# Performance work log

Measured on AMD Instinct MI355X. Metric: run time of the kernel, lower is better.

## Reference

```python
import jax, jax.numpy as jnp
import numpy as np

B, T, H, D = 2, 2048, 8, 128
HID = H * D          # 1024
K_CONV = 4
EPS = 1e-5


def causal_dwconv(x, w, b):
    # x: [B,T,C], w: [C,K], b: [C]
    # torch Conv1d(groups=C, padding=K-1) followed by [..., :T] == left-padded causal depthwise conv
    K = w.shape[1]
    Tx = x.shape[1]
    xp = jnp.pad(x, ((0, 0), (K - 1, 0), (0, 0)))
    acc = jnp.zeros_like(x)
    for j in range(K):  # tiny fixed loop over kernel taps
        acc = acc + xp[:, j:j + Tx, :] * w[:, j]
    return acc + b


def setup_inputs() -> dict:
    key = jax.random.key(0)
    ks = jax.random.split(key, 16)
    s = 0.02
    inp = {
        'x':   jax.random.normal(ks[0], (B, T, HID), jnp.float32),
        'Wq':  s * jax.random.normal(ks[1], (HID, H * D), jnp.float32),
        'Wk':  s * jax.random.normal(ks[2], (HID, H * D), jnp.float32),
        'Wv':  s * jax.random.normal(ks[3], (HID, H * D), jnp.float32),
        'Wa':  s * jax.random.normal(ks[4], (HID, H * D), jnp.float32),
        'ba':  jnp.zeros((H * D,), jnp.float32),
        'Wb':  s * jax.random.normal(ks[5], (HID, H), jnp.float32),
        'bb':  jnp.zeros((H,), jnp.float32),
        'Wg':  s * jax.random.normal(ks[6], (HID, H * D), jnp.float32),
        'Wo':  s * jax.random.normal(ks[7], (H * D, HID), jnp.float32),
        'cqw': s * jax.random.normal(ks[8], (H * D, K_CONV), jnp.float32),
        'cqb': jnp.zeros((H * D,), jnp.float32),
        'ckw': s * jax.random.normal(ks[9], (H * D, K_CONV), jnp.float32),
        'ckb': jnp.zeros((H * D,), jnp.float32),
        'cvw': s * jax.random.normal(ks[10], (H * D, K_CONV), jnp.float32),
        'cvb': jnp.zeros((H * D,), jnp.float32),
        'ln_g': jnp.ones((D,), jnp.float32),
        'ln_b': jnp.zeros((D,), jnp.float32),
    }
    return inp


def reference(x, Wq, Wk, Wv, Wa, ba, Wb, bb, Wg, Wo,
              cqw, cqb, ckw, ckb, cvw, cvb, ln_g, ln_b):
    Bx, Tx, _ = x.shape
    q = x @ Wq
    k = x @ Wk
    v = x @ Wv
    q = jax.nn.silu(causal_dwconv(q, cqw, cqb))
    k = jax.nn.silu(causal_dwconv(k, ckw, ckb))
    v = jax.nn.silu(causal_dwconv(v, cvw, cvb))
    q = q.reshape(Bx, Tx, H, D)
    k = k.reshape(Bx, Tx, H, D) * (D ** -0.5)   # k scaled by head_dim_qk**-0.5
    v = v.reshape(Bx, Tx, H, D)
    a = jax.nn.sigmoid(x @ Wa + ba).reshape(Bx, Tx, H, D)
    beta = jax.nn.sigmoid(x @ Wb + bb)           # [B,T,H]

    # delta-rule recurrent scan; state S: [B,H,Dv,Dk]
    def step(S, inp):
        q_t, k_t, v_t, a_t, b_t = inp            # [B,H,D] / beta [B,H]
        delta = jnp.einsum('bhvk,bhk->bhv', S, k_t)
        err = delta - v_t
        S = a_t[..., None] * S - (b_t[..., None] * err)[..., None] * k_t[:, :, None, :]
        o_t = jnp.einsum('bhvk,bhk->bhv', S, q_t)
        return S, o_t

    tfirst = lambda z: jnp.moveaxis(z, 1, 0)     # [B,T,...] -> [T,B,...]
    S0 = jnp.zeros((Bx, H, D, D), x.dtype)
    _, o = jax.lax.scan(step, S0, (tfirst(q), tfirst(k), tfirst(v), tfirst(a), tfirst(beta)))
    o = jnp.moveaxis(o, 0, 1)                    # [B,T,H,D]

    # LayerNorm over head_dim_v
    mu = o.mean(-1, keepdims=True)
    var = ((o - mu) ** 2).mean(-1, keepdims=True)
    o = (o - mu) * jax.lax.rsqrt(var + EPS) * ln_g + ln_b

    g = jax.nn.sigmoid(x @ Wg).reshape(Bx, Tx, H, D)
    o = (o * g).reshape(Bx, Tx, H * D)
    return o @ Wo
```

## Files before the change

### kernel.cpp

```cpp
#include <hip/hip_runtime.h>
#include <hip/hip_bf16.h>
#include <cstdint>
#include <cstddef>

#define BATCH 2
#define TLEN  2048
#define NHEAD 8
#define HD    128
#define HIDN  1024
#define MTOT  4096
#define MAT_ELEMS 1048576
#define XELEMS 4194304
#define SCAN_C 32
#define NCH    64
#define SSC  1024.0f
#define ISSC 0.0009765625f

typedef _Float16 f16;
typedef _Float16 f16x2 __attribute__((ext_vector_type(2)));
typedef _Float16 f16x8 __attribute__((ext_vector_type(8)));
typedef float    f32x4 __attribute__((ext_vector_type(4)));

__device__ __forceinline__ float sigmoidf_(float v) { return 1.0f / (1.0f + __expf(-v)); }

__device__ __forceinline__ float fdot2_(f16x2 a, f16x2 b, float c)
{
#if __has_builtin(__builtin_amdgcn_fdot2)
    return __builtin_amdgcn_fdot2(a, b, c, false);
#else
    return fmaf((float)a.x, (float)b.x, fmaf((float)a.y, (float)b.y, c));
#endif
}

__device__ __forceinline__ void gload_lds16(const f16* g, f16* l)
{
    __builtin_amdgcn_global_load_lds(
        (const __attribute__((address_space(1))) uint32_t*)(g),
        (__attribute__((address_space(3))) uint32_t*)(l), 16, 0, 0);
}

__global__ __launch_bounds__(256) void convert_x_kernel(const float* __restrict__ x,
                                                        f16* __restrict__ x16)
{
    int i = (blockIdx.x * 256 + threadIdx.x) * 4;
    float4 v = *(const float4*)(x + i);
    union { f16 h[4]; uint2 u; } pk;
    pk.h[0] = (f16)v.x; pk.h[1] = (f16)v.y; pk.h[2] = (f16)v.z; pk.h[3] = (f16)v.w;
    *(uint2*)(x16 + i) = pk.u;
}

__global__ __launch_bounds__(256) void transpose_convert_kernel(
    const float* __restrict__ Wq, const float* __restrict__ Wk, const float* __restrict__ Wv,
    const float* __restrict__ Wa, const float* __restrict__ Wg, const float* __restrict__ Wo,
    f16* __restrict__ WT)
{
    __shared__ float tile[32][33];
    int mat = blockIdx.z;
    const float* W = (mat == 0) ? Wq : (mat == 1) ? Wk : (mat == 2) ? Wv
                   : (mat == 3) ? Wa : (mat == 4) ? Wg : Wo;
    int k0 = blockIdx.y * 32, n0 = blockIdx.x * 32;
    int tr = threadIdx.x >> 3;
    int tc = (threadIdx.x & 7) * 4;
    float4 vin = *(const float4*)(W + (size_t)(k0 + tr) * HIDN + n0 + tc);
    tile[tr][tc + 0] = vin.x; tile[tr][tc + 1] = vin.y;
    tile[tr][tc + 2] = vin.z; tile[tr][tc + 3] = vin.w;
    __syncthreads();
    f16* dst = WT + (size_t)(mat * HIDN + n0 + tr) * HIDN + k0 + tc;
    union { f16 h[4]; uint2 u; } pk;
    pk.h[0] = (f16)tile[tc + 0][tr]; pk.h[1] = (f16)tile[tc + 1][tr];
    pk.h[2] = (f16)tile[tc + 2][tr]; pk.h[3] = (f16)tile[tc + 3][tr];
    *(uint2*)dst = pk.u;
}

template <int MODE>
__global__ __launch_bounds__(256) void gemm_f16(
    const f16* __restrict__ A, const f16* __restrict__ BT,
    float* __restrict__ out_f32,
    f16* __restrict__ qkv_hat, float* __restrict__ a_buf, f16* __restrict__ g16,
    const float* __restrict__ ba)
{
    __shared__ __align__(16) f16 As[128][32];
    __shared__ __align__(16) f16 Bs[128][32];
    int m0 = blockIdx.y * 128;
    int n0 = blockIdx.x * 128;
    int tid = threadIdx.x;
    int w = tid >> 6, lane = tid & 63;
    int L16 = lane & 15, quad = lane >> 4;
    int wm = (w >> 1) * 64, wn = (w & 1) * 64;

    f32x4 acc[4][4];
#pragma unroll
    for (int i = 0; i < 4; ++i)
#pragma unroll
        for (int j = 0; j < 4; ++j) acc[i][j] = (f32x4){0.f, 0.f, 0.f, 0.f};

    int ldr = tid >> 2;
    int ldc = (tid & 3) * 8;
    f16* asb0 = &As[0][0]  + w * 512;
    f16* asb1 = &As[64][0] + w * 512;
    f16* bsb0 = &Bs[0][0]  + w * 512;
    f16* bsb1 = &Bs[64][0] + w * 512;

    for (int k0 = 0; k0 < 1024; k0 += 32) {
        __syncthreads();
        gload_lds16(A  + (size_t)(m0 + ldr) * HIDN + k0 + ldc,      asb0);
        gload_lds16(A  + (size_t)(m0 + ldr + 64) * HIDN + k0 + ldc, asb1);
        gload_lds16(BT + (size_t)(n0 + ldr) * HIDN + k0 + ldc,      bsb0);
        gload_lds16(BT + (size_t)(n0 + ldr + 64) * HIDN + k0 + ldc, bsb1);
        __syncthreads();
        f16x8 af[4], bf[4];
#pragma unroll
        for (int i = 0; i < 4; ++i) {
            af[i] = *(const f16x8*)(&As[wm + i * 16 + L16][quad * 8]);
            bf[i] = *(const f16x8*)(&Bs[wn + i * 16 + L16][quad * 8]);
        }
#pragma unroll
        for (int i = 0; i < 4; ++i)
#pragma unroll
            for (int j = 0; j < 4; ++j)
                acc[i][j] = __builtin_amdgcn_mfma_f32_16x16x32_f16(af[i], bf[j], acc[i][j], 0, 0, 0);
    }

#pragma unroll
    for (int i = 0; i < 4; ++i) {
#pragma unroll
        for (int j = 0; j < 4; ++j) {
            f32x4 c = acc[i][j];
            int mbase = m0 + wm + i * 16 + quad * 4;
            int n = n0 + wn + j * 16 + L16;
            if (MODE == 1) {
#pragma unroll
                for (int r = 0; r < 4; ++r)
                    out_f32[(size_t)(mbase + r) * HIDN + n] = c[r];
            } else {
                int mat = n >> 10;
                int nn = n & 1023;
                if (mat < 3) {
#pragma unroll
                    for (int r = 0; r < 4; ++r)
                        qkv_hat[(size_t)mat * XELEMS + (size_t)(mbase + r) * HIDN + nn] = (f16)c[r];
                } else if (mat == 3) {
                    float bav = ba[nn];
#pragma unroll
                    for (int r = 0; r < 4; ++r)
                        a_buf[(size_t)(mbase + r) * HIDN + nn] = sigmoidf_(c[r] + bav);
                } else {
#pragma unroll
                    for (int r = 0; r < 4; ++r)
                        g16[(size_t)(mbase + r) * HIDN + nn] = (f16)sigmoidf_(c[r]);
                }
            }
        }
    }
}

__global__ __launch_bounds__(256) void beta_kernel(const float* __restrict__ x,
                                                   const float* __restrict__ Wb,
                                                   const float* __restrict__ bb,
                                                   float* __restrict__ beta_buf)
{
    int row = blockIdx.x;
    int h = threadIdx.x >> 5, lane = threadIdx.x & 31;
    const float* xr = x + (size_t)row * HIDN;
    float part = 0.f;
    for (int i = lane; i < HIDN; i += 32)
        part += xr[i] * Wb[i * NHEAD + h];
#pragma unroll
    for (int m = 1; m <= 16; m <<= 1) part += __shfl_xor(part, m);
    if (lane == 0)
        beta_buf[(size_t)row * NHEAD + h] = sigmoidf_(part + bb[h]);
}

__global__ __launch_bounds__(256) void conv_silu_kernel(
    const f16* __restrict__ qkv_hat,
    const float* __restrict__ cqw, const float* __restrict__ cqb,
    const float* __restrict__ ckw, const float* __restrict__ ckb,
    const float* __restrict__ cvw, const float* __restrict__ cvb,
    f16* __restrict__ qkv16)
{
    int z = blockIdx.y;
    int row = blockIdx.x;
    int tloc = row & (TLEN - 1);
    int c4 = threadIdx.x * 4;
    const f16* src = qkv_hat + (size_t)z * XELEMS;
    const float* w  = (z == 0) ? cqw : (z == 1) ? ckw : cvw;
    const float* bi = (z == 0) ? cqb : (z == 1) ? ckb : cvb;

    float xv[4][4];
#pragma unroll
    for (int j = 0; j < 4; ++j) {
        int tt = tloc - 3 + j;
        if (tt >= 0) {
            const f16* p = src + (size_t)(row - 3 + j) * HIDN + c4;
            xv[j][0] = (float)p[0]; xv[j][1] = (float)p[1];
            xv[j][2] = (float)p[2]; xv[j][3] = (float)p[3];
        } else {
            xv[j][0] = xv[j][1] = xv[j][2] = xv[j][3] = 0.f;
        }
    }
    float scale = (z == 1) ? 0.08838834764831845f : 1.0f;
    union { f16 h[4]; uint2 u; } pk;
#pragma unroll
    for (int cc = 0; cc < 4; ++cc) {
        float4 wc = *(const float4*)(w + (size_t)(c4 + cc) * 4);
        float acc = bi[c4 + cc] + wc.x * xv[0][cc] + wc.y * xv[1][cc]
                                 + wc.z * xv[2][cc] + wc.w * xv[3][cc];
        pk.h[cc] = (f16)(acc * sigmoidf_(acc) * scale);
    }
    *(uint2*)(qkv16 + (size_t)z * XELEMS + (size_t)row * HIDN + c4) = pk.u;
}

__global__ __launch_bounds__(64) void gram_kernel(
    const f16* __restrict__ q16, const f16* __restrict__ k16,
    f16* __restrict__ G_g, f16* __restrict__ KQ_g,
    f16* __restrict__ Gx_g, f16* __restrict__ Qx_g, f16* __restrict__ KT_g)
{
    int ch = blockIdx.x;
    int bh = blockIdx.y;
    int b = bh >> 3, h = bh & 7;
    int lane = threadIdx.x;
    int L16 = lane & 15, quad = lane >> 4;
    size_t rowbase = (size_t)(b * TLEN) * HIDN + h * HD;
    int t0 = ch * SCAN_C;
    bool hasNext = (ch + 1 < NCH);

    union ZU { uint4 u; f16x8 v; };
    ZU zz; zz.u = (uint4){0, 0, 0, 0};

    f16x8 kc[2][4], qc[2][4], kn[2][4], qn[2][4];
#pragma unroll
    for (int nt = 0; nt < 2; ++nt)
#pragma unroll
        for (int kk = 0; kk < 4; ++kk) {
            size_t g = rowbase + (size_t)(t0 + nt * 16 + L16) * HIDN + kk * 32 + quad * 8;
            kc[nt][kk] = *(const f16x8*)(k16 + g);
            qc[nt][kk] = *(const f16x8*)(q16 + g);
            if (hasNext) {
                kn[nt][kk] = *(const f16x8*)(k16 + g + (size_t)SCAN_C * HIDN);
                qn[nt][kk] = *(const f16x8*)(q16 + g + (size_t)SCAN_C * HIDN);
            } else {
                kn[nt][kk] = zz.v; qn[nt][kk] = zz.v;
            }
        }

    f32x4 aG[2][2], aKQ[2][2], aGx[2][2], aQx[2][2];
#pragma unroll
    for (int i = 0; i < 2; ++i)
#pragma unroll
        for (int j = 0; j < 2; ++j) {
            aG[i][j] = (f32x4){0, 0, 0, 0}; aKQ[i][j] = (f32x4){0, 0, 0, 0};
            aGx[i][j] = (f32x4){0, 0, 0, 0}; aQx[i][j] = (f32x4){0, 0, 0, 0};
        }
#pragma unroll
    for (int kk = 0; kk < 4; ++kk)
#pragma unroll
        for (int mt = 0; mt < 2; ++mt)
#pragma unroll
            for (int nt = 0; nt < 2; ++nt) {
                aG[mt][nt]  = __builtin_amdgcn_mfma_f32_16x16x32_f16(kc[mt][kk], kc[nt][kk], aG[mt][nt], 0, 0, 0);
                aKQ[mt][nt] = __builtin_amdgcn_mfma_f32_16x16x32_f16(kc[mt][kk], qc[nt][kk], aKQ[mt][nt], 0, 0, 0);
                aGx[mt][nt] = __builtin_amdgcn_mfma_f32_16x16x32_f16(kc[mt][kk], kn[nt][kk], aGx[mt][nt], 0, 0, 0);
                aQx[mt][nt] = __builtin_amdgcn_mfma_f32_16x16x32_f16(kc[mt][kk], qn[nt][kk], aQx[mt][nt], 0, 0, 0);
            }

    size_t gb = ((size_t)bh * NCH + ch) * 1024;
#pragma unroll
    for (int nt = 0; nt < 2; ++nt) {
        int t = nt * 16 + L16;
#pragma unroll
        for (int mt = 0; mt < 2; ++mt) {
            union { f16 e[4]; uint2 u2; } pg, pq, px, py;
#pragma unroll
            for (int r = 0; r < 4; ++r) {
                pg.e[r] = (f16)aG[mt][nt][r];
                pq.e[r] = (f16)aKQ[mt][nt][r];
                px.e[r] = (f16)aGx[mt][nt][r];
                py.e[r] = (f16)aQx[mt][nt][r];
            }
            *(uint2*)(G_g  + gb + t * 32 + mt * 16 + quad * 4) = pg.u2;
            *(uint2*)(KQ_g + gb + t * 32 + mt * 16 + quad * 4) = pq.u2;
            *(uint2*)(Gx_g + gb + t * 32 + mt * 16 + quad * 4) = px.u2;
            *(uint2*)(Qx_g + gb + t * 32 + mt * 16 + quad * 4) = py.u2;
        }
    }
    size_t kb = ((size_t)bh * NCH + ch) * 4096;
#pragma unroll
    for (int nt = 0; nt < 2; ++nt) {
        int t = nt * 16 + L16;
#pragma unroll
        for (int kk = 0; kk < 4; ++kk)
#pragma unroll
            for (int j = 0; j < 8; ++j) {
                int k = kk * 32 + quad * 8 + j;
                KT_g[kb + (size_t)k * 32 + t] = kc[nt][kk][j];
            }
    }
}

__global__ __launch_bounds__(128, 1) void scan2_kernel(
    const f16* __restrict__ q16, const f16* __restrict__ k16, const f16* __restrict__ v16,
    const float* __restrict__ a_buf, const float* __restrict__ beta_buf,
    const f16* __restrict__ G_g, const f16* __restrict__ KQ_g,
    const f16* __restrict__ Gx_g, const f16* __restrict__ Qx_g, const f16* __restrict__ KT_g,
    float* __restrict__ o_buf)
{
    __shared__ __align__(16) float Sp[16 * 132];
    __shared__ __align__(16) f16   Sp16[16 * 136];
    __shared__ __align__(16) f16   KT_lds2[2][4096];
    __shared__ __align__(16) f16   G_lds[2][1024];
    __shared__ __align__(16) f16   Q_lds[2][1024];
    __shared__ __align__(16) f16   Gx_lds[2][1024];
    __shared__ __align__(16) f16   Qx_lds[2][1024];
    __shared__ __align__(16) float skv[2][16 * 34];
    __shared__ __align__(16) float sqv[2][16 * 34];
    __shared__ __align__(16) float avb[2][16 * 68];
    __shared__ __align__(16) float Bts[2][32];
    __shared__ __align__(16) f16   c16s[2][16 * 40];
    __shared__ __align__(16) float PCs[2][16];
    __shared__ __align__(16) float o_lds[2][16][34];

    const int tid = threadIdx.x;
    const int wid = tid >> 6;
    const int lane = tid & 63;
    const int L16 = lane & 15, quad = lane >> 4;
    const int vl = lane >> 2, li = lane & 3;
    const int t_av = lane >> 1, halfsel = lane & 1;

    const int bh = blockIdx.x;
    const int b = bh >> 3, h = bh & 7;
    const int v0 = blockIdx.y * 16;
    const size_t rowbase = (size_t)(b * TLEN) * HIDN + h * HD;
    const size_t gmatbase = (size_t)bh * NCH;

    {
        for (int i = tid; i < 16 * 132; i += 128) Sp[i] = 0.f;
        uint32_t* z;
        z = (uint32_t*)Sp16;    for (int i = tid; i < 16 * 136 / 2; i += 128) z[i] = 0u;
        z = (uint32_t*)KT_lds2; for (int i = tid; i < 2 * 4096 / 2; i += 128) z[i] = 0u;
        z = (uint32_t*)G_lds;   for (int i = tid; i < 1024;          i += 128) z[i] = 0u;
        z = (uint32_t*)Q_lds;   for (int i = tid; i < 1024;          i += 128) z[i] = 0u;
        z = (uint32_t*)Gx_lds;  for (int i = tid; i < 1024;          i += 128) z[i] = 0u;
        z = (uint32_t*)Qx_lds;  for (int i = tid; i < 1024;          i += 128) z[i] = 0u;
        z = (uint32_t*)skv;     for (int i = tid; i < 2 * 16 * 34;   i += 128) z[i] = 0u;
        z = (uint32_t*)sqv;     for (int i = tid; i < 2 * 16 * 34;   i += 128) z[i] = 0u;
        z = (uint32_t*)avb;     for (int i = tid; i < 2 * 16 * 68;   i += 128) z[i] = 0u;
        z = (uint32_t*)Bts;     for (int i = tid; i < 2 * 32;        i += 128) z[i] = 0u;
        z = (uint32_t*)c16s;    for (int i = tid; i < 2 * 16 * 40 / 2; i += 128) z[i] = 0u;
        z = (uint32_t*)PCs;     for (int i = tid; i < 2 * 16;        i += 128) z[i] = 0u;
    }
    __syncthreads();

    if (wid == 1) {
        f16x8 kfA[2][4], qfA[2][4], kfB[2][4], qfB[2][4];

        {
            size_t gb0 = gmatbase * 1024;
            *(uint4*)(&G_lds[0][lane * 16])     = *(const uint4*)(G_g  + gb0 + lane * 16);
            *(uint4*)(&G_lds[0][lane * 16 + 8]) = *(const uint4*)(G_g  + gb0 + lane * 16 + 8);
            *(uint4*)(&Q_lds[0][lane * 16])     = *(const uint4*)(KQ_g + gb0 + lane * 16);
            *(uint4*)(&Q_lds[0][lane * 16 + 8]) = *(const uint4*)(KQ_g + gb0 + lane * 16 + 8);
            size_t ga = rowbase + (size_t)t_av * HIDN + v0 + halfsel * 8;
            float4 ar0 = *(const float4*)(a_buf + ga);
            float4 ar1 = *(const float4*)(a_buf + ga + 4);
            uint4  vr  = *(const uint4*)(v16 + ga);
            float betr = beta_buf[((size_t)(b * TLEN) + t_av) * NHEAD + h];
            const f16* vh = (const f16*)&vr;
            const float* aa0 = (const float*)&ar0;
            const float* aa1 = (const float*)&ar1;
#pragma unroll
            for (int e = 0; e < 4; ++e) {
                float2 wv; wv.x = aa0[e]; wv.y = betr * (float)vh[e];
                *(float2*)(&avb[0][(halfsel * 8 + e) * 68 + 2 * t_av]) = wv;
                float2 wu; wu.x = aa1[e]; wu.y = betr * (float)vh[4 + e];
                *(float2*)(&avb[0][(halfsel * 8 + 4 + e) * 68 + 2 * t_av]) = wu;
            }
            if (halfsel == 0) Bts[0][t_av] = betr;
        }
        __syncthreads();

#define DO_UPDATE_MM(KF, QF)                                                        \
        if (ch >= 1 && ch <= NCH - 2) {                                             \
            f16x8 ca = *(const f16x8*)(&c16s[np][L16 * 40 + quad * 8]);             \
            float pc = PCs[np][L16];                                                \
            _Pragma("unroll")                                                       \
            for (int kt = 0; kt < 8; ++kt) {                                        \
                f16x8 bu = *(const f16x8*)(&KT_lds2[p][(kt * 16 + L16) * 32 + quad * 8]); \
                f32x4 d = __builtin_amdgcn_mfma_f32_16x16x32_f16(bu, ca, (f32x4){0, 0, 0, 0}, 0, 0, 0); \
                int idx = L16 * 132 + kt * 16 + quad * 4;                           \
                float4 s = *(const float4*)(&Sp[idx]);                              \
                s.x = fmaf(pc, s.x, d[0]);                                          \
                s.y = fmaf(pc, s.y, d[1]);                                          \
                s.z = fmaf(pc, s.z, d[2]);                                          \
                s.w = fmaf(pc, s.w, d[3]);                                          \
                *(float4*)(&Sp[idx]) = s;                                           \
                union { f16 e[4]; uint2 u2; } ph;                                   \
                ph.e[0] = (f16)s.x; ph.e[1] = (f16)s.y;                             \
                ph.e[2] = (f16)s.z; ph.e[3] = (f16)s.w;                             \
                *(uint2*)(&Sp16[L16 * 136 + kt * 16 + quad * 4]) = ph.u2;           \
            }                                                                       \
            f32x4 accK[2], accQ[2];                                                 \
            accK[0] = (f32x4){0, 0, 0, 0}; accK[1] = (f32x4){0, 0, 0, 0};           \
            accQ[0] = (f32x4){0, 0, 0, 0}; accQ[1] = (f32x4){0, 0, 0, 0};           \
            _Pragma("unroll")                                                       \
            for (int kk = 0; kk < 4; ++kk) {                                        \
                f16x8 sf = *(const f16x8*)(&Sp16[L16 * 136 + kk * 32 + quad * 8]);  \
                _Pragma("unroll")                                                   \
                for (int nt = 0; nt < 2; ++nt) {                                    \
                    accK[nt] = __builtin_amdgcn_mfma_f32_16x16x32_f16(sf, KF[nt][kk], accK[nt], 0, 0, 0); \
                    accQ[nt] = __builtin_amdgcn_mfma_f32_16x16x32_f16(sf, QF[nt][kk], accQ[nt], 0, 0, 0); \
                }                                                                   \
            }                                                                       \
            _Pragma("unroll")                                                       \
            for (int nt = 0; nt < 2; ++nt) {                                        \
                int t = nt * 16 + L16;                                              \
                _Pragma("unroll")                                                   \
                for (int r = 0; r < 4; ++r) {                                       \
                    skv[np][(quad * 4 + r) * 34 + t] = accK[nt][r];                 \
                    sqv[np][(quad * 4 + r) * 34 + t] = accQ[nt][r];                 \
                }                                                                   \
            }                                                                       \
        }

#define DO_PREFETCH(KF, QF)                                                         \
        if (ch <= NCH - 3) {                                                        \
            int tp = (ch + 2) * SCAN_C;                                             \
            _Pragma("unroll")                                                       \
            for (int nt = 0; nt < 2; ++nt)                                          \
                _Pragma("unroll")                                                   \
                for (int kk = 0; kk < 4; ++kk) {                                    \
                    size_t g = rowbase + (size_t)(tp + nt * 16 + L16) * HIDN + kk * 32 + quad * 8; \
                    KF[nt][kk] = *(const f16x8*)(k16 + g);                          \
                    QF[nt][kk] = *(const f16x8*)(q16 + g);                          \
                }                                                                   \
        }

        for (int ch = 0; ch < NCH; ++ch) {
            const int p = ch & 1;
            const int np = p ^ 1;
            const bool haveNext = (ch + 1 < NCH);

            float4 ar0, ar1; uint4 vr; float betr = 0.f;
            if (haveNext) {
                size_t gbn = (gmatbase + ch + 1) * 1024;
                size_t gbc = (gmatbase + ch) * 1024;
                const f16* gG = G_g  + gbn + lane * 8;
                const f16* gQ = KQ_g + gbn + lane * 8;
                const f16* gX = Gx_g + gbc + lane * 8;
                const f16* gY = Qx_g + gbc + lane * 8;
                gload_lds16(gG,       &G_lds[np][0]);
                gload_lds16(gG + 512, &G_lds[np][512]);
                gload_lds16(gQ,       &Q_lds[np][0]);
                gload_lds16(gQ + 512, &Q_lds[np][512]);
                gload_lds16(gX,       &Gx_lds[np][0]);
                gload_lds16(gX + 512, &Gx_lds[np][512]);
                gload_lds16(gY,       &Qx_lds[np][0]);
                gload_lds16(gY + 512, &Qx_lds[np][512]);
                const f16* gK = KT_g + (gmatbase + ch) * 4096 + lane * 8;
#pragma unroll
                for (int i = 0; i < 8; ++i)
                    gload_lds16(gK + i * 512, &KT_lds2[np][i * 512]);
                int tn = (ch + 1) * SCAN_C;
                size_t ga = rowbase + (size_t)(tn + t_av) * HIDN + v0 + halfsel * 8;
                ar0 = *(const float4*)(a_buf + ga);
                ar1 = *(const float4*)(a_buf + ga + 4);
                vr  = *(const uint4*)(v16 + ga);
                betr = beta_buf[((size_t)(b * TLEN) + tn + t_av) * NHEAD + h];
            }

            if ((ch & 1) == 0) { DO_PREFETCH(kfB, qfB) }
            else               { DO_PREFETCH(kfA, qfA) }

            if (ch >= 1) {
                const int fp = (ch - 1) & 1;
                const int tprev = (ch - 1) * SCAN_C;
                const int tt = lane >> 1;
                const int hh = (lane & 1) * 8;
                float v8[8];
#pragma unroll
                for (int j = 0; j < 8; ++j) v8[j] = o_lds[fp][hh + j][tt];
                float4 f0; f0.x = v8[0]; f0.y = v8[1]; f0.z = v8[2]; f0.w = v8[3];
                float4 f1; f1.x = v8[4]; f1.y = v8[5]; f1.z = v8[6]; f1.w = v8[7];
                size_t ob = rowbase + (size_t)(tprev + tt) * HIDN + v0 + hh;
                *(float4*)(o_buf + ob)     = f0;
                *(float4*)(o_buf + ob + 4) = f1;
            }

            if ((ch & 1) == 0) { DO_UPDATE_MM(kfA, qfA) }
            else               { DO_UPDATE_MM(kfB, qfB) }

            if (haveNext) {
                const f16* vh = (const f16*)&vr;
                const float* aa0 = (const float*)&ar0;
                const float* aa1 = (const float*)&ar1;
#pragma unroll
                for (int e = 0; e < 4; ++e) {
                    float2 wv; wv.x = aa0[e]; wv.y = betr * (float)vh[e];
                    *(float2*)(&avb[np][(halfsel * 8 + e) * 68 + 2 * t_av]) = wv;
                    float2 wu; wu.x = aa1[e]; wu.y = betr * (float)vh[4 + e];
                    *(float2*)(&avb[np][(halfsel * 8 + 4 + e) * 68 + 2 * t_av]) = wu;
                }
                if (halfsel == 0) Bts[np][t_av] = betr;
            }
            __syncthreads();
        }
#undef DO_UPDATE_MM
#undef DO_PREFETCH

        {
            const int fp = (NCH - 1) & 1;
            const int tprev = (NCH - 1) * SCAN_C;
            const int tt = lane >> 1;
            const int hh = (lane & 1) * 8;
            float v8[8];
#pragma unroll
            for (int j = 0; j < 8; ++j) v8[j] = o_lds[fp][hh + j][tt];
            float4 f0; f0.x = v8[0]; f0.y = v8[1]; f0.z = v8[2]; f0.w = v8[3];
            float4 f1; f1.x = v8[4]; f1.y = v8[5]; f1.z = v8[6]; f1.w = v8[7];
            size_t ob = rowbase + (size_t)(tprev + tt) * HIDN + v0 + hh;
            *(float4*)(o_buf + ob)     = f0;
            *(float4*)(o_buf + ob + 4) = f1;
        }
    } else {
        __builtin_amdgcn_s_setprio(1);
        __syncthreads();

        for (int ch = 0; ch < NCH; ++ch) {
            const int p = ch & 1;
            const int np = p ^ 1;

            {
                f16x8 caf = *(const f16x8*)(&c16s[np][L16 * 40 + quad * 8]);
                f32x4 fK[2], fQ[2];
#pragma unroll
                for (int nt = 0; nt < 2; ++nt) {
                    f16x8 bx = *(const f16x8*)(&Gx_lds[p][(nt * 16 + L16) * 32 + quad * 8]);
                    f16x8 by = *(const f16x8*)(&Qx_lds[p][(nt * 16 + L16) * 32 + quad * 8]);
                    fK[nt] = __builtin_amdgcn_mfma_f32_16x16x32_f16(caf, bx, (f32x4){0, 0, 0, 0}, 0, 0, 0);
                    fQ[nt] = __builtin_amdgcn_mfma_f32_16x16x32_f16(caf, by, (f32x4){0, 0, 0, 0}, 0, 0, 0);
                }
#pragma unroll
                for (int r = 0; r < 4; ++r) {
                    int vv = quad * 4 + r;
                    float Pv = PCs[np][vv];
#pragma unroll
                    for (int nt = 0; nt < 2; ++nt) {
                        int t = nt * 16 + L16;
                        skv[p][vv * 34 + t] = fmaf(Pv, skv[p][vv * 34 + t], fK[nt][r]);
                        sqv[p][vv * 34 + t] = fmaf(Pv, sqv[p][vv * 34 + t], fQ[nt][r]);
                    }
                }
            }

            {
                f16x2 c0, c1, c2, c3;
                c0.x = (f16)0.f; c0.y = (f16)0.f; c1 = c0; c2 = c0; c3 = c0;
                float P = 1.f;
                union RowU { uint4 u4; f16x2 h2[4]; };

#pragma unroll
                for (int wnd = 0; wnd < 4; ++wnd) {
                    const int tw = wnd * 8;
                    uint4  bg0[4], bg1[4], bh0[4], bh1[4];
                    float2 bskp[4], bsqp[4], bbtp[4];
                    float4 bab4[4];
                    float  bkq00[4], bg01[4];
                    f16x2  bdq[4];
#pragma unroll
                    for (int i = 0; i < 4; ++i) {
                        const int t = tw + i * 2;
                        bg0[i] = *(const uint4*)(&G_lds[p][t * 32 + li * 8]);
                        bg1[i] = *(const uint4*)(&G_lds[p][(t + 1) * 32 + li * 8]);
                        bh0[i] = *(const uint4*)(&Q_lds[p][t * 32 + li * 8]);
                        bh1[i] = *(const uint4*)(&Q_lds[p][(t + 1) * 32 + li * 8]);
                        bskp[i] = *(const float2*)(&skv[p][vl * 34 + t]);
                        bsqp[i] = *(const float2*)(&sqv[p][vl * 34 + t]);
                        bab4[i] = *(const float4*)(&avb[p][vl * 68 + 2 * t]);
                        bbtp[i] = *(const float2*)(&Bts[p][t]);
                        bkq00[i] = (float)Q_lds[p][t * 32 + t];
                        bdq[i]  = *(const f16x2*)(&Q_lds[p][(t + 1) * 32 + t]);
                        bg01[i] = (float)G_lds[p][(t + 1) * 32 + t];
                    }
#pragma unroll
                    for (int i = 0; i < 4; ++i) {
                        const int t = tw + i * 2;
                        RowU g0u, g1u, h0u, h1u;
                        g0u.u4 = bg0[i]; g1u.u4 = bg1[i];
                        h0u.u4 = bh0[i]; h1u.u4 = bh1[i];
                        float2 skp = bskp[i], sqp = bsqp[i], btp = bbtp[i];
                        float4 ab4 = bab4[i];
                        float kq00 = bkq00[i], g01 = bg01[i];
                        f16x2 dq = bdq[i];

                        float pG  = fdot2_(c0, g0u.h2[0], fdot2_(c1, g0u.h2[1], 0.f))
                                  + fdot2_(c2, g0u.h2[2], fdot2_(c3, g0u.h2[3], 0.f));
                        float pG1 = fdot2_(c0, g1u.h2[0], fdot2_(c1, g1u.h2[1], 0.f))
                                  + fdot2_(c2, g1u.h2[2], fdot2_(c3, g1u.h2[3], 0.f));
                        float pO  = fdot2_(c0, h0u.h2[0], fdot2_(c1, h0u.h2[1], 0.f))
                                  + fdot2_(c2, h0u.h2[2], fdot2_(c3, h0u.h2[3], 0.f));
                        float pO1 = fdot2_(c0, h1u.h2[0], fdot2_(c1, h1u.h2[1], 0.f))
                                  + fdot2_(c2, h1u.h2[2], fdot2_(c3, h1u.h2[3], 0.f));
                        int tmp;
                        tmp = __builtin_amdgcn_update_dpp(0, __float_as_int(pG),  0xB1, 0xF, 0xF, true); pG  += __int_as_float(tmp);
                        tmp = __builtin_amdgcn_update_dpp(0, __float_as_int(pG1), 0xB1, 0xF, 0xF, true); pG1 += __int_as_float(tmp);
                        tmp = __builtin_amdgcn_update_dpp(0, __float_as_int(pO),  0xB1, 0xF, 0xF, true); pO  += __int_as_float(tmp);
                        tmp = __builtin_amdgcn_update_dpp(0, __float_as_int(pO1), 0xB1, 0xF, 0xF, true); pO1 += __int_as_float(tmp);
                        tmp = __builtin_amdgcn_update_dpp(0, __float_as_int(pG),  0x4E, 0xF, 0xF, true); pG  += __int_as_float(tmp);
                        tmp = __builtin_amdgcn_update_dpp(0, __float_as_int(pG1), 0x4E, 0xF, 0xF, true); pG1 += __int_as_float(tmp);
                        tmp = __builtin_amdgcn_update_dpp(0, __float_as_int(pO),  0x4E, 0xF, 0xF, true); pO  += __int_as_float(tmp);
                        tmp = __builtin_amdgcn_update_dpp(0, __float_as_int(pO1), 0x4E, 0xF, 0xF, true); pO1 += __int_as_float(tmp);

                        float a0 = ab4.x, bv0 = ab4.y, a1 = ab4.z, bv1 = ab4.w;
                        float bt0 = btp.x, bt1 = btp.y;
                        float sk0 = skp.x * ISSC, sk1 = skp.y * ISSC;
                        float sq0 = sqp.x * ISSC, sq1 = sqp.y * ISSC;
                        float kq01 = (float)dq.x, kq11 = (float)dq.y;

                        float x0 = fmaf(P, sk0, pG);
                        float u0 = fmaf(-bt0, x0, bv0);
                        float P0 = P * a0;
                        float o0 = fmaf(a0, pO, u0 * kq00);
                        o0 = fmaf(P0, sq0, o0);
                        float accGv = fmaf(a0, pG1, u0 * g01);
                        float x1 = fmaf(P0, sk1, accGv);
                        float u1 = fmaf(-bt1, x1, bv1);
                        float P1 = P0 * a1;
                        float accOv = fmaf(a0, pO1, u0 * kq01);
                        float o1 = fmaf(a1, accOv, u1 * kq11);
                        o1 = fmaf(P1, sq1, o1);

                        float aa = a0 * a1;
                        f16 aah = (f16)aa;
                        f16x2 aa2; aa2.x = aah; aa2.y = aah;
                        c0 *= aa2; c1 *= aa2; c2 *= aa2; c3 *= aa2;
                        if (li == (t >> 3)) {
                            f16x2 un; un.x = (f16)(u0 * a1); un.y = (f16)u1;
                            int sel = (t & 7) >> 1;
                            if (sel == 0) c0 = un; else if (sel == 1) c1 = un;
                            else if (sel == 2) c2 = un; else c3 = un;
                        }
                        P = P1;
                        if (li == 0) {
                            float2 o2; o2.x = o0; o2.y = o1;
                            *(float2*)(&o_lds[p][vl][t]) = o2;
                        }
                    }
                }
                f16 s16 = (f16)SSC;
                f16x2 ss2; ss2.x = s16; ss2.y = s16;
                union { f16x2 h2[4]; uint4 u4; } pc;
                pc.h2[0] = c0 * ss2; pc.h2[1] = c1 * ss2; pc.h2[2] = c2 * ss2; pc.h2[3] = c3 * ss2;
                *(uint4*)(&c16s[p][vl * 40 + li * 8]) = pc.u4;
                if (li == 0) PCs[p][vl] = P;
            }
            __syncthreads();
        }
    }
}

__global__ __launch_bounds__(256) void ln_gate_kernel(
    const float* __restrict__ o_buf, const f16* __restrict__ g16,
    const float* __restrict__ lng, const float* __restrict__ lnb,
    f16* __restrict__ og16)
{
    int row = blockIdx.x;
    int h = threadIdx.x >> 5, lane = threadIdx.x & 31;
    size_t base = (size_t)row * HIDN + h * HD + lane * 4;
    float4 x = *(const float4*)(o_buf + base);
    float s  = x.x + x.y + x.z + x.w;
    float sq = x.x * x.x + x.y * x.y + x.z * x.z + x.w * x.w;
#pragma unroll
    for (int m = 1; m <= 16; m <<= 1) {
        s  += __shfl_xor(s, m);
        sq += __shfl_xor(sq, m);
    }
    float mu  = s * (1.0f / 128.0f);
    float var = sq * (1.0f / 128.0f) - mu * mu;
    float inv = 1.0f / sqrtf(var + 1e-5f);
    int d = lane * 4;
    const float* xp = (const float*)&x;
    union { f16 h4[4]; uint2 u; } pk;
#pragma unroll
    for (int j = 0; j < 4; ++j) {
        float on = (xp[j] - mu) * inv * lng[d + j] + lnb[d + j];
        pk.h4[j] = (f16)(on * (float)g16[base + j]);
    }
    *(uint2*)(og16 + base) = pk.u;
}

extern "C" void kernel_launch(void* const* d_in, const int* in_sizes, int n_in,
                              void* d_out, int out_size, void* d_ws, size_t ws_size,
                              hipStream_t stream)
{
    (void)in_sizes; (void)n_in; (void)out_size; (void)ws_size;
    const float* x   = (const float*)d_in[0];
    const float* Wq  = (const float*)d_in[1];
    const float* Wk  = (const float*)d_in[2];
    const float* Wv  = (const float*)d_in[3];
    const float* Wa  = (const float*)d_in[4];
    const float* ba  = (const float*)d_in[5];
    const float* Wb  = (const float*)d_in[6];
    const float* bb  = (const float*)d_in[7];
    const float* Wg  = (const float*)d_in[8];
    const float* Wo  = (const float*)d_in[9];
    const float* cqw = (const float*)d_in[10];
    const float* cqb = (const float*)d_in[11];
    const float* ckw = (const float*)d_in[12];
    const float* ckb = (const float*)d_in[13];
    const float* cvw = (const float*)d_in[14];
    const float* cvb = (const float*)d_in[15];
    const float* lng = (const float*)d_in[16];
    const float* lnb = (const float*)d_in[17];
    float* out = (float*)d_out;

    char* ws = (char*)d_ws;
    f16*   x16      = (f16*)(ws + 0);
    f16*   WT       = (f16*)(ws + 8388608);
    f16*   qkvh     = (f16*)(ws + 20971520);
    f16*   qkv16    = (f16*)(ws + 46137344);
    float* a_buf    = (float*)(ws + 96468992);
    f16*   g16      = (f16*)(ws + 113246208);
    float* beta_buf = (float*)(ws + 121634816);
    float* o_buf    = (float*)(ws + 121765888);
    f16*   og16     = (f16*)(ws + 138543104);

    f16* G_g  = qkvh;
    f16* KQ_g = qkvh + 1048576;
    f16* Gx_g = qkvh + 2097152;
    f16* Qx_g = qkvh + 3145728;
    f16* KT_g = qkvh + 4194304;

    convert_x_kernel<<<dim3(4096), dim3(256), 0, stream>>>(x, x16);
    transpose_convert_kernel<<<dim3(32, 32, 6), dim3(256), 0, stream>>>(Wq, Wk, Wv, Wa, Wg, Wo, WT);
    gemm_f16<0><<<dim3(40, 32), dim3(256), 0, stream>>>(x16, WT, nullptr, qkvh, a_buf, g16, ba);
    beta_kernel<<<dim3(4096), dim3(256), 0, stream>>>(x, Wb, bb, beta_buf);
    conv_silu_kernel<<<dim3(4096, 3), dim3(256), 0, stream>>>(qkvh, cqw, cqb, ckw, ckb, cvw, cvb, qkv16);
    gram_kernel<<<dim3(NCH, 16), dim3(64), 0, stream>>>(
        qkv16, qkv16 + XELEMS, G_g, KQ_g, Gx_g, Qx_g, KT_g);
    scan2_kernel<<<dim3(16, 8), dim3(128), 0, stream>>>(
        qkv16, qkv16 + XELEMS, qkv16 + 2 * (size_t)XELEMS, a_buf, beta_buf,
        G_g, KQ_g, Gx_g, Qx_g, KT_g, o_buf);
    ln_gate_kernel<<<dim3(4096), dim3(256), 0, stream>>>(o_buf, g16, lng, lnb, og16);
    gemm_f16<1><<<dim3(8, 32), dim3(256), 0, stream>>>(og16, WT + 5 * (size_t)MAT_ELEMS, out,
                                                       nullptr, nullptr, nullptr, nullptr);
}
```

Measured before the change: 515.4 us.

## Pack four value-slices per scan block and move state and KT operands to registers

The scan kernel now runs four independent 16-column value slices per 512-thread block (grid 16x2 instead of 16x8), each pair of waves using its own LDS partition, so the per-chunk G/KQ tiles are shared per block load pattern and fewer blocks exist. The fp32 state tile is kept in registers instead of LDS, KT operands are loaded straight from global into registers, and Gx/Qx fragments are register-prefetched one chunk ahead, which removes several LDS buffers and async copies. The intent is to reduce LDS traffic and per-chunk copy latency on the serial recurrence. The cost is that all four slices now synchronise on block-wide barriers, and there are fewer blocks (32) across the CUs, with higher register pressure.

```diff
diff --git a/kernel.cpp b/kernel.cpp
--- a/kernel.cpp
+++ b/kernel.cpp
@@ -297,68 +297,67 @@
     }
 }
 
-__global__ __launch_bounds__(128, 1) void scan2_kernel(
+__global__ __launch_bounds__(512, 2) void scan2_kernel(
     const f16* __restrict__ q16, const f16* __restrict__ k16, const f16* __restrict__ v16,
     const float* __restrict__ a_buf, const float* __restrict__ beta_buf,
     const f16* __restrict__ G_g, const f16* __restrict__ KQ_g,
     const f16* __restrict__ Gx_g, const f16* __restrict__ Qx_g, const f16* __restrict__ KT_g,
     float* __restrict__ o_buf)
 {
-    __shared__ __align__(16) float Sp[16 * 132];
-    __shared__ __align__(16) f16   Sp16[16 * 136];
-    __shared__ __align__(16) f16   KT_lds2[2][4096];
-    __shared__ __align__(16) f16   G_lds[2][1024];
-    __shared__ __align__(16) f16   Q_lds[2][1024];
-    __shared__ __align__(16) f16   Gx_lds[2][1024];
-    __shared__ __align__(16) f16   Qx_lds[2][1024];
-    __shared__ __align__(16) float skv[2][16 * 34];
-    __shared__ __align__(16) float sqv[2][16 * 34];
-    __shared__ __align__(16) float avb[2][16 * 68];
-    __shared__ __align__(16) float Bts[2][32];
-    __shared__ __align__(16) f16   c16s[2][16 * 40];
-    __shared__ __align__(16) float PCs[2][16];
-    __shared__ __align__(16) float o_lds[2][16][34];
+    __shared__ __align__(16) f16   Sp16_a[4][16 * 136];
+    __shared__ __align__(16) f16   G_a[4][2][1024];
+    __shared__ __align__(16) f16   Q_a[4][2][1024];
+    __shared__ __align__(16) float skv_a[4][2][16 * 34];
+    __shared__ __align__(16) float sqv_a[4][2][16 * 34];
+    __shared__ __align__(16) float avb_a[4][2][16 * 68];
+    __shared__ __align__(16) float Bts_a[4][2][32];
+    __shared__ __align__(16) f16   c16s_a[4][2][16 * 40];
+    __shared__ __align__(16) float PCs_a[4][2][16];
+    __shared__ __align__(16) float o_a[4][2][16][34];
 
     const int tid = threadIdx.x;
     const int wid = tid >> 6;
     const int lane = tid & 63;
+    const int pp = wid >> 1;
+    const int role = wid & 1;
+    const int ptid = (role << 6) | lane;
     const int L16 = lane & 15, quad = lane >> 4;
     const int vl = lane >> 2, li = lane & 3;
     const int t_av = lane >> 1, halfsel = lane & 1;
 
     const int bh = blockIdx.x;
     const int b = bh >> 3, h = bh & 7;
-    const int v0 = blockIdx.y * 16;
+    const int v0 = (blockIdx.y * 4 + pp) * 16;
     const size_t rowbase = (size_t)(b * TLEN) * HIDN + h * HD;
     const size_t gmatbase = (size_t)bh * NCH;
 
     {
-        for (int i = tid; i < 16 * 132; i += 128) Sp[i] = 0.f;
         uint32_t* z;
-        z = (uint32_t*)Sp16;    for (int i = tid; i < 16 * 136 / 2; i += 128) z[i] = 0u;
-        z = (uint32_t*)KT_lds2; for (int i = tid; i < 2 * 4096 / 2; i += 128) z[i] = 0u;
-        z = (uint32_t*)G_lds;   for (int i = tid; i < 1024;          i += 128) z[i] = 0u;
-        z = (uint32_t*)Q_lds;   for (int i = tid; i < 1024;          i += 128) z[i] = 0u;
-        z = (uint32_t*)Gx_lds;  for (int i = tid; i < 1024;          i += 128) z[i] = 0u;
-        z = (uint32_t*)Qx_lds;  for (int i = tid; i < 1024;          i += 128) z[i] = 0u;
-        z = (uint32_t*)skv;     for (int i = tid; i < 2 * 16 * 34;   i += 128) z[i] = 0u;
-        z = (uint32_t*)sqv;     for (int i = tid; i < 2 * 16 * 34;   i += 128) z[i] = 0u;
-        z = (uint32_t*)avb;     for (int i = tid; i < 2 * 16 * 68;   i += 128) z[i] = 0u;
-        z = (uint32_t*)Bts;     for (int i = tid; i < 2 * 32;        i += 128) z[i] = 0u;
-        z = (uint32_t*)c16s;    for (int i = tid; i < 2 * 16 * 40 / 2; i += 128) z[i] = 0u;
-        z = (uint32_t*)PCs;     for (int i = tid; i < 2 * 16;        i += 128) z[i] = 0u;
+        z = (uint32_t*)&Sp16_a[pp][0];      for (int i = ptid; i < 16 * 136 / 2;   i += 128) z[i] = 0u;
+        z = (uint32_t*)&G_a[pp][0][0];      for (int i = ptid; i < 2 * 1024 / 2;   i += 128) z[i] = 0u;
+        z = (uint32_t*)&Q_a[pp][0][0];      for (int i = ptid; i < 2 * 1024 / 2;   i += 128) z[i] = 0u;
+        z = (uint32_t*)&skv_a[pp][0][0];    for (int i = ptid; i < 2 * 16 * 34;    i += 128) z[i] = 0u;
+        z = (uint32_t*)&sqv_a[pp][0][0];    for (int i = ptid; i < 2 * 16 * 34;    i += 128) z[i] = 0u;
+        z = (uint32_t*)&avb_a[pp][0][0];    for (int i = ptid; i < 2 * 16 * 68;    i += 128) z[i] = 0u;
+        z = (uint32_t*)&Bts_a[pp][0][0];    for (int i = ptid; i < 2 * 32;         i += 128) z[i] = 0u;
+        z = (uint32_t*)&c16s_a[pp][0][0];   for (int i = ptid; i < 2 * 16 * 40 / 2; i += 128) z[i] = 0u;
+        z = (uint32_t*)&PCs_a[pp][0][0];    for (int i = ptid; i < 2 * 16;         i += 128) z[i] = 0u;
+        z = (uint32_t*)&o_a[pp][0][0][0];   for (int i = ptid; i < 2 * 16 * 34;    i += 128) z[i] = 0u;
     }
     __syncthreads();
 
-    if (wid == 1) {
+    if (role == 1) {
         f16x8 kfA[2][4], qfA[2][4], kfB[2][4], qfB[2][4];
+        f32x4 sreg[8];
+#pragma unroll
+        for (int i = 0; i < 8; ++i) sreg[i] = (f32x4){0.f, 0.f, 0.f, 0.f};
 
         {
             size_t gb0 = gmatbase * 1024;
-            *(uint4*)(&G_lds[0][lane * 16])     = *(const uint4*)(G_g  + gb0 + lane * 16);
-            *(uint4*)(&G_lds[0][lane * 16 + 8]) = *(const uint4*)(G_g  + gb0 + lane * 16 + 8);
-            *(uint4*)(&Q_lds[0][lane * 16])     = *(const uint4*)(KQ_g + gb0 + lane * 16);
-            *(uint4*)(&Q_lds[0][lane * 16 + 8]) = *(const uint4*)(KQ_g + gb0 + lane * 16 + 8);
+            *(uint4*)(&G_a[pp][0][lane * 16])     = *(const uint4*)(G_g  + gb0 + lane * 16);
+            *(uint4*)(&G_a[pp][0][lane * 16 + 8]) = *(const uint4*)(G_g  + gb0 + lane * 16 + 8);
+            *(uint4*)(&Q_a[pp][0][lane * 16])     = *(const uint4*)(KQ_g + gb0 + lane * 16);
+            *(uint4*)(&Q_a[pp][0][lane * 16 + 8]) = *(const uint4*)(KQ_g + gb0 + lane * 16 + 8);
             size_t ga = rowbase + (size_t)t_av * HIDN + v0 + halfsel * 8;
             float4 ar0 = *(const float4*)(a_buf + ga);
             float4 ar1 = *(const float4*)(a_buf + ga + 4);
@@ -370,40 +369,43 @@
 #pragma unroll
             for (int e = 0; e < 4; ++e) {
                 float2 wv; wv.x = aa0[e]; wv.y = betr * (float)vh[e];
-                *(float2*)(&avb[0][(halfsel * 8 + e) * 68 + 2 * t_av]) = wv;
+                *(float2*)(&avb_a[pp][0][(halfsel * 8 + e) * 68 + 2 * t_av]) = wv;
                 float2 wu; wu.x = aa1[e]; wu.y = betr * (float)vh[4 + e];
-                *(float2*)(&avb[0][(halfsel * 8 + 4 + e) * 68 + 2 * t_av]) = wu;
-            }
-            if (halfsel == 0) Bts[0][t_av] = betr;
+                *(float2*)(&avb_a[pp][0][(halfsel * 8 + 4 + e) * 68 + 2 * t_av]) = wu;
+            }
+            if (halfsel == 0) Bts_a[pp][0][t_av] = betr;
         }
         __syncthreads();
 
 #define DO_UPDATE_MM(KF, QF)                                                        \
         if (ch >= 1 && ch <= NCH - 2) {                                             \
-            f16x8 ca = *(const f16x8*)(&c16s[np][L16 * 40 + quad * 8]);             \
-            float pc = PCs[np][L16];                                                \
+            f16x8 ca = *(const f16x8*)(&c16s_a[pp][np][L16 * 40 + quad * 8]);       \
+            float pc = PCs_a[pp][np][L16];                                          \
+            const f16* ktb = KT_g + ((size_t)gmatbase + ch - 1) * 4096 + (size_t)L16 * 32 + quad * 8; \
+            f16x8 bu[8];                                                            \
+            _Pragma("unroll")                                                       \
+            for (int kt = 0; kt < 8; ++kt)                                          \
+                bu[kt] = *(const f16x8*)(ktb + (size_t)kt * 512);                   \
             _Pragma("unroll")                                                       \
             for (int kt = 0; kt < 8; ++kt) {                                        \
-                f16x8 bu = *(const f16x8*)(&KT_lds2[p][(kt * 16 + L16) * 32 + quad * 8]); \
-                f32x4 d = __builtin_amdgcn_mfma_f32_16x16x32_f16(bu, ca, (f32x4){0, 0, 0, 0}, 0, 0, 0); \
-                int idx = L16 * 132 + kt * 16 + quad * 4;                           \
-                float4 s = *(const float4*)(&Sp[idx]);                              \
+                f32x4 d = __builtin_amdgcn_mfma_f32_16x16x32_f16(bu[kt], ca, (f32x4){0, 0, 0, 0}, 0, 0, 0); \
+                f32x4 s = sreg[kt];                                                 \
                 s.x = fmaf(pc, s.x, d[0]);                                          \
                 s.y = fmaf(pc, s.y, d[1]);                                          \
                 s.z = fmaf(pc, s.z, d[2]);                                          \
                 s.w = fmaf(pc, s.w, d[3]);                                          \
-                *(float4*)(&Sp[idx]) = s;                                           \
+                sreg[kt] = s;                                                       \
                 union { f16 e[4]; uint2 u2; } ph;                                   \
                 ph.e[0] = (f16)s.x; ph.e[1] = (f16)s.y;                             \
                 ph.e[2] = (f16)s.z; ph.e[3] = (f16)s.w;                             \
-                *(uint2*)(&Sp16[L16 * 136 + kt * 16 + quad * 4]) = ph.u2;           \
+                *(uint2*)(&Sp16_a[pp][L16 * 136 + kt * 16 + quad * 4]) = ph.u2;     \
             }                                                                       \
             f32x4 accK[2], accQ[2];                                                 \
             accK[0] = (f32x4){0, 0, 0, 0}; accK[1] = (f32x4){0, 0, 0, 0};           \
             accQ[0] = (f32x4){0, 0, 0, 0}; accQ[1] = (f32x4){0, 0, 0, 0};           \
             _Pragma("unroll")                                                       \
             for (int kk = 0; kk < 4; ++kk) {                                        \
-                f16x8 sf = *(const f16x8*)(&Sp16[L16 * 136 + kk * 32 + quad * 8]);  \
+                f16x8 sf = *(const f16x8*)(&Sp16_a[pp][L16 * 136 + kk * 32 + quad * 8]); \
                 _Pragma("unroll")                                                   \
                 for (int nt = 0; nt < 2; ++nt) {                                    \
                     accK[nt] = __builtin_amdgcn_mfma_f32_16x16x32_f16(sf, KF[nt][kk], accK[nt], 0, 0, 0); \
@@ -415,8 +417,8 @@
                 int t = nt * 16 + L16;                                              \
                 _Pragma("unroll")                                                   \
                 for (int r = 0; r < 4; ++r) {                                       \
-                    skv[np][(quad * 4 + r) * 34 + t] = accK[nt][r];                 \
-                    sqv[np][(quad * 4 + r) * 34 + t] = accQ[nt][r];                 \
+                    skv_a[pp][np][(quad * 4 + r) * 34 + t] = accK[nt][r];           \
+                    sqv_a[pp][np][(quad * 4 + r) * 34 + t] = accQ[nt][r];           \
                 }                                                                   \
             }                                                                       \
         }
@@ -442,23 +444,12 @@
             float4 ar0, ar1; uint4 vr; float betr = 0.f;
             if (haveNext) {
                 size_t gbn = (gmatbase + ch + 1) * 1024;
-                size_t gbc = (gmatbase + ch) * 1024;
                 const f16* gG = G_g  + gbn + lane * 8;
                 const f16* gQ = KQ_g + gbn + lane * 8;
-                const f16* gX = Gx_g + gbc + lane * 8;
-                const f16* gY = Qx_g + gbc + lane * 8;
-                gload_lds16(gG,       &G_lds[np][0]);
-                gload_lds16(gG + 512, &G_lds[np][512]);
-                gload_lds16(gQ,       &Q_lds[np][0]);
-                gload_lds16(gQ + 512, &Q_lds[np][512]);
-                gload_lds16(gX,       &Gx_lds[np][0]);
-                gload_lds16(gX + 512, &Gx_lds[np][512]);
-                gload_lds16(gY,       &Qx_lds[np][0]);
-                gload_lds16(gY + 512, &Qx_lds[np][512]);
-                const f16* gK = KT_g + (gmatbase + ch) * 4096 + lane * 8;
-#pragma unroll
-                for (int i = 0; i < 8; ++i)
-                    gload_lds16(gK + i * 512, &KT_lds2[np][i * 512]);
+                gload_lds16(gG,       &G_a[pp][np][0]);
+                gload_lds16(gG + 512, &G_a[pp][np][512]);
+                gload_lds16(gQ,       &Q_a[pp][np][0]);
+                gload_lds16(gQ + 512, &Q_a[pp][np][512]);
                 int tn = (ch + 1) * SCAN_C;
                 size_t ga = rowbase + (size_t)(tn + t_av) * HIDN + v0 + halfsel * 8;
                 ar0 = *(const float4*)(a_buf + ga);
@@ -477,7 +468,7 @@
                 const int hh = (lane & 1) * 8;
                 float v8[8];
 #pragma unroll
-                for (int j = 0; j < 8; ++j) v8[j] = o_lds[fp][hh + j][tt];
+                for (int j = 0; j < 8; ++j) v8[j] = o_a[pp][fp][hh + j][tt];
                 float4 f0; f0.x = v8[0]; f0.y = v8[1]; f0.z = v8[2]; f0.w = v8[3];
                 float4 f1; f1.x = v8[4]; f1.y = v8[5]; f1.z = v8[6]; f1.w = v8[7];
                 size_t ob = rowbase + (size_t)(tprev + tt) * HIDN + v0 + hh;
@@ -495,11 +486,11 @@
 #pragma unroll
                 for (int e = 0; e < 4; ++e) {
                     float2 wv; wv.x = aa0[e]; wv.y = betr * (float)vh[e];
-                    *(float2*)(&avb[np][(halfsel * 8 + e) * 68 + 2 * t_av]) = wv;
+                    *(float2*)(&avb_a[pp][np][(halfsel * 8 + e) * 68 + 2 * t_av]) = wv;
                     float2 wu; wu.x = aa1[e]; wu.y = betr * (float)vh[4 + e];
-                    *(float2*)(&avb[np][(halfsel * 8 + 4 + e) * 68 + 2 * t_av]) = wu;
+                    *(float2*)(&avb_a[pp][np][(halfsel * 8 + 4 + e) * 68 + 2 * t_av]) = wu;
                 }
-                if (halfsel == 0) Bts[np][t_av] = betr;
+                if (halfsel == 0) Bts_a[pp][np][t_av] = betr;
             }
             __syncthreads();
         }
@@ -513,7 +504,7 @@
             const int hh = (lane & 1) * 8;
             float v8[8];
 #pragma unroll
-            for (int j = 0; j < 8; ++j) v8[j] = o_lds[fp][hh + j][tt];
+            for (int j = 0; j < 8; ++j) v8[j] = o_a[pp][fp][hh + j][tt];
             float4 f0; f0.x = v8[0]; f0.y = v8[1]; f0.z = v8[2]; f0.w = v8[3];
             float4 f1; f1.x = v8[4]; f1.y = v8[5]; f1.z = v8[6]; f1.w = v8[7];
             size_t ob = rowbase + (size_t)(tprev + tt) * HIDN + v0 + hh;
@@ -521,6 +512,13 @@
             *(float4*)(o_buf + ob + 4) = f1;
         }
     } else {
+        f16x8 bxA[2], byA[2], bxB[2], byB[2];
+#pragma unroll
+        for (int nt = 0; nt < 2; ++nt) {
+            size_t gx0 = (size_t)gmatbase * 1024 + (size_t)(nt * 16 + L16) * 32 + quad * 8;
+            bxA[nt] = *(const f16x8*)(Gx_g + gx0);
+            byA[nt] = *(const f16x8*)(Qx_g + gx0);
+        }
         __builtin_amdgcn_s_setprio(1);
         __syncthreads();
 
@@ -529,25 +527,34 @@
             const int np = p ^ 1;
 
             {
-                f16x8 caf = *(const f16x8*)(&c16s[np][L16 * 40 + quad * 8]);
+                f16x8 caf = *(const f16x8*)(&c16s_a[pp][np][L16 * 40 + quad * 8]);
                 f32x4 fK[2], fQ[2];
 #pragma unroll
                 for (int nt = 0; nt < 2; ++nt) {
-                    f16x8 bx = *(const f16x8*)(&Gx_lds[p][(nt * 16 + L16) * 32 + quad * 8]);
-                    f16x8 by = *(const f16x8*)(&Qx_lds[p][(nt * 16 + L16) * 32 + quad * 8]);
+                    f16x8 bx = (p == 0) ? bxA[nt] : bxB[nt];
+                    f16x8 by = (p == 0) ? byA[nt] : byB[nt];
                     fK[nt] = __builtin_amdgcn_mfma_f32_16x16x32_f16(caf, bx, (f32x4){0, 0, 0, 0}, 0, 0, 0);
                     fQ[nt] = __builtin_amdgcn_mfma_f32_16x16x32_f16(caf, by, (f32x4){0, 0, 0, 0}, 0, 0, 0);
                 }
 #pragma unroll
                 for (int r = 0; r < 4; ++r) {
                     int vv = quad * 4 + r;
-                    float Pv = PCs[np][vv];
+                    float Pv = PCs_a[pp][np][vv];
 #pragma unroll
                     for (int nt = 0; nt < 2; ++nt) {
                         int t = nt * 16 + L16;
-                        skv[p][vv * 34 + t] = fmaf(Pv, skv[p][vv * 34 + t], fK[nt][r]);
-                        sqv[p][vv * 34 + t] = fmaf(Pv, sqv[p][vv * 34 + t], fQ[nt][r]);
+                        skv_a[pp][p][vv * 34 + t] = fmaf(Pv, skv_a[pp][p][vv * 34 + t], fK[nt][r]);
+                        sqv_a[pp][p][vv * 34 + t] = fmaf(Pv, sqv_a[pp][p][vv * 34 + t], fQ[nt][r]);
                     }
+                }
+            }
+
+            if (ch + 1 < NCH) {
+#pragma unroll
+                for (int nt = 0; nt < 2; ++nt) {
+                    size_t gxn = ((size_t)gmatbase + ch) * 1024 + (size_t)(nt * 16 + L16) * 32 + quad * 8;
+                    if (p == 0) { bxB[nt] = *(const f16x8*)(Gx_g + gxn); byB[nt] = *(const f16x8*)(Qx_g + gxn); }
+                    else        { bxA[nt] = *(const f16x8*)(Gx_g + gxn); byA[nt] = *(const f16x8*)(Qx_g + gxn); }
                 }
             }
 
@@ -568,17 +575,17 @@
 #pragma unroll
                     for (int i = 0; i < 4; ++i) {
                         const int t = tw + i * 2;
-                        bg0[i] = *(const uint4*)(&G_lds[p][t * 32 + li * 8]);
-                        bg1[i] = *(const uint4*)(&G_lds[p][(t + 1) * 32 + li * 8]);
-                        bh0[i] = *(const uint4*)(&Q_lds[p][t * 32 + li * 8]);
-                        bh1[i] = *(const uint4*)(&Q_lds[p][(t + 1) * 32 + li * 8]);
-                        bskp[i] = *(const float2*)(&skv[p][vl * 34 + t]);
-                        bsqp[i] = *(const float2*)(&sqv[p][vl * 34 + t]);
-                        bab4[i] = *(const float4*)(&avb[p][vl * 68 + 2 * t]);
-                        bbtp[i] = *(const float2*)(&Bts[p][t]);
-                        bkq00[i] = (float)Q_lds[p][t * 32 + t];
-                        bdq[i]  = *(const f16x2*)(&Q_lds[p][(t + 1) * 32 + t]);
-                        bg01[i] = (float)G_lds[p][(t + 1) * 32 + t];
+                        bg0[i] = *(const uint4*)(&G_a[pp][p][t * 32 + li * 8]);
+                        bg1[i] = *(const uint4*)(&G_a[pp][p][(t + 1) * 32 + li * 8]);
+                        bh0[i] = *(const uint4*)(&Q_a[pp][p][t * 32 + li * 8]);
+                        bh1[i] = *(const uint4*)(&Q_a[pp][p][(t + 1) * 32 + li * 8]);
+                        bskp[i] = *(const float2*)(&skv_a[pp][p][vl * 34 + t]);
+                        bsqp[i] = *(const float2*)(&sqv_a[pp][p][vl * 34 + t]);
+                        bab4[i] = *(const float4*)(&avb_a[pp][p][vl * 68 + 2 * t]);
+                        bbtp[i] = *(const float2*)(&Bts_a[pp][p][t]);
+                        bkq00[i] = (float)Q_a[pp][p][t * 32 + t];
+                        bdq[i]  = *(const f16x2*)(&Q_a[pp][p][(t + 1) * 32 + t]);
+                        bg01[i] = (float)G_a[pp][p][(t + 1) * 32 + t];
                     }
 #pragma unroll
                     for (int i = 0; i < 4; ++i) {
@@ -641,7 +648,7 @@
                         P = P1;
                         if (li == 0) {
                             float2 o2; o2.x = o0; o2.y = o1;
-                            *(float2*)(&o_lds[p][vl][t]) = o2;
+                            *(float2*)(&o_a[pp][p][vl][t]) = o2;
                         }
                     }
                 }
@@ -649,8 +656,8 @@
                 f16x2 ss2; ss2.x = s16; ss2.y = s16;
                 union { f16x2 h2[4]; uint4 u4; } pc;
                 pc.h2[0] = c0 * ss2; pc.h2[1] = c1 * ss2; pc.h2[2] = c2 * ss2; pc.h2[3] = c3 * ss2;
-                *(uint4*)(&c16s[p][vl * 40 + li * 8]) = pc.u4;
-                if (li == 0) PCs[p][vl] = P;
+                *(uint4*)(&c16s_a[pp][p][vl * 40 + li * 8]) = pc.u4;
+                if (li == 0) PCs_a[pp][p][vl] = P;
             }
             __syncthreads();
         }
@@ -736,7 +743,7 @@
     conv_silu_kernel<<<dim3(4096, 3), dim3(256), 0, stream>>>(qkvh, cqw, cqb, ckw, ckb, cvw, cvb, qkv16);
     gram_kernel<<<dim3(NCH, 16), dim3(64), 0, stream>>>(
         qkv16, qkv16 + XELEMS, G_g, KQ_g, Gx_g, Qx_g, KT_g);
-    scan2_kernel<<<dim3(16, 8), dim3(128), 0, stream>>>(
+    scan2_kernel<<<dim3(16, 2), dim3(512), 0, stream>>>(
         qkv16, qkv16 + XELEMS, qkv16 + 2 * (size_t)XELEMS, a_buf, beta_buf,
         G_g, KQ_g, Gx_g, Qx_g, KT_g, o_buf);
     ln_gate_kernel<<<dim3(4096), dim3(256), 0, stream>>>(o_buf, g16, lng, lnb, og16);
```

New measurement: 718.7 us. 39.4% more time.
